# Performance work log

Hardware: AMD Instinct MI355X
Metric: run time of the kernel (lower is better)

The kernel has to match this reference:

```python
import jax, jax.numpy as jnp
import numpy as np

B, S, HID = 1, 2048, 2880
H, KV, D = 64, 8, 64
WINDOW = 128
SCALE = D ** -0.5
NEG_INF = jnp.float32(-1e30)


def _rope_cos_sin():
    # realistic RoPE tables over full head_dim (HF rotate_half convention)
    inv_freq = 1.0 / (10000.0 ** (np.arange(0, D, 2, dtype=np.float32) / D))
    t = np.arange(S, dtype=np.float32)
    freqs = np.outer(t, inv_freq)                      # [S, D/2]
    emb = np.concatenate([freqs, freqs], axis=-1)      # [S, D]
    return jnp.asarray(np.cos(emb))[None], jnp.asarray(np.sin(emb))[None]


def setup_inputs() -> dict:
    key = jax.random.key(0)
    ks = jax.random.split(key, 10)
    cos, sin = _rope_cos_sin()
    sd = lambda fan_in: 1.0 / np.sqrt(fan_in)
    return {
        "hidden_states": jax.random.normal(ks[0], (B, S, HID), jnp.float32),
        "cos": cos, "sin": sin,
        "Wq": jax.random.normal(ks[1], (HID, H * D), jnp.float32) * sd(HID),
        "bq": jax.random.normal(ks[2], (H * D,), jnp.float32) * 0.02,
        "Wk": jax.random.normal(ks[3], (HID, KV * D), jnp.float32) * sd(HID),
        "bk": jax.random.normal(ks[4], (KV * D,), jnp.float32) * 0.02,
        "Wv": jax.random.normal(ks[5], (HID, KV * D), jnp.float32) * sd(HID),
        "bv": jax.random.normal(ks[6], (KV * D,), jnp.float32) * 0.02,
        "Wo": jax.random.normal(ks[7], (H * D, HID), jnp.float32) * sd(H * D),
        "bo": jax.random.normal(ks[8], (HID,), jnp.float32) * 0.02,
        "sinks": jax.random.normal(ks[9], (H,), jnp.float32),
    }


def _rotate_half(x):
    x1, x2 = jnp.split(x, 2, axis=-1)
    return jnp.concatenate([-x2, x1], axis=-1)


def _forward(hidden_states, cos, sin, Wq, bq, Wk, bk, Wv, bv, Wo, bo, sinks):
    q = (hidden_states @ Wq + bq).reshape(B, S, H, D)
    k = (hidden_states @ Wk + bk).reshape(B, S, KV, D)
    v = (hidden_states @ Wv + bv).reshape(B, S, KV, D)
    # RoPE with explicit cos/sin, unsqueeze at head dim (bsnd layout)
    c, s = cos[:, :, None, :], sin[:, :, None, :]
    q = q * c + _rotate_half(q) * s
    k = k * c + _rotate_half(k) * s
    # GQA: expand kv heads to match query heads
    k = jnp.repeat(k, H // KV, axis=2)
    v = jnp.repeat(v, H // KV, axis=2)
    scores = jnp.einsum("bqhd,bkhd->bhqk", q, k) * SCALE  # [B,H,S,S]
    i = jnp.arange(S)[:, None]
    j = jnp.arange(S)[None, :]
    allowed = (j <= i) & (j > i - WINDOW)                  # causal + sliding window
    scores = jnp.where(allowed, scores, NEG_INF)
    # sink-augmented softmax: sinks act as an extra logit per head, dropped after norm
    m = jnp.maximum(scores.max(axis=-1), sinks[None, :, None])  # [B,H,S]
    p = jnp.exp(scores - m[..., None])                      # [B,H,S,S]
    denom = p.sum(axis=-1) + jnp.exp(sinks[None, :, None] - m)  # [B,H,S]
    attn = jnp.einsum("bhqk,bkhd->bqhd", p, v) / denom.transpose(0, 2, 1)[..., None]
    return attn.reshape(B, S, H * D) @ Wo + bo


def reference(hidden_states, cos, sin, Wq, bq, Wk, bk, Wv, bv, Wo, bo, sinks):
    return _forward(hidden_states, cos, sin, Wq, bq, Wk, bk, Wv, bv, Wo, bo, sinks)
```

## Files before the change

### kernel.cpp

```cpp
#include <hip/hip_runtime.h>

typedef unsigned short u16;
typedef __bf16 bf16x8 __attribute__((ext_vector_type(8)));
typedef float f32x4 __attribute__((ext_vector_type(4)));

constexpr int SEQ = 2048;
constexpr int HIDN = 2880;
constexpr int NQKV = 5120;
constexpr float SCALE = 0.125f;
constexpr float NEG_INF = -1e30f;

#define ASM_VMCNT(n)  asm volatile("s_waitcnt vmcnt(" #n ")" ::: "memory")
#define ASM_LGKM(n)   asm volatile("s_waitcnt lgkmcnt(" #n ")" ::: "memory")
#define ASM_BARRIER() asm volatile("s_barrier" ::: "memory")
#define SCHEDBAR()    __builtin_amdgcn_sched_barrier(0)

__device__ __forceinline__ u16 f2bf(float f) {
  unsigned int u = __builtin_bit_cast(unsigned int, f);
  u += 0x7FFFu + ((u >> 16) & 1u);
  return (u16)(u >> 16);
}
__device__ __forceinline__ float bf2f(u16 h) {
  unsigned int u = ((unsigned int)h) << 16;
  return __builtin_bit_cast(float, u);
}
__device__ __forceinline__ void async_load16(const void* g, void* l) {
  __builtin_amdgcn_global_load_lds(
      (const __attribute__((address_space(1))) unsigned int*)g,
      (__attribute__((address_space(3))) unsigned int*)l, 16, 0, 0);
}
__device__ __forceinline__ f32x4 DSR(unsigned addr) {
  f32x4 d;
  asm volatile("ds_read_b128 %0, %1" : "=v"(d) : "v"(addr));
  return d;
}
__device__ __forceinline__ bf16x8 asbf(f32x4 v) { return __builtin_bit_cast(bf16x8, v); }

__global__ __launch_bounds__(256) void conv_f2b(const float* __restrict__ in,
                                                u16* __restrict__ out, long n4) {
  long i = (long)blockIdx.x * 256 + threadIdx.x;
  if (i >= n4) return;
  float4 v = ((const float4*)in)[i];
  u16 o0 = f2bf(v.x), o1 = f2bf(v.y), o2 = f2bf(v.z), o3 = f2bf(v.w);
  out[i * 4 + 0] = o0; out[i * 4 + 1] = o1; out[i * 4 + 2] = o2; out[i * 4 + 3] = o3;
}

__global__ __launch_bounds__(256) void transpose_qkv(const float* __restrict__ Wq,
                                                     const float* __restrict__ Wk,
                                                     const float* __restrict__ Wv,
                                                     u16* __restrict__ out) {
  __shared__ float tile[32][33];
  int c0 = blockIdx.x * 32, r0 = blockIdx.y * 32;
  int tx = threadIdx.x & 31, ty = threadIdx.x >> 5;
  const float* src; int C, cl;
  if (c0 < 4096)      { src = Wq; C = 4096; cl = c0; }
  else if (c0 < 4608) { src = Wk; C = 512;  cl = c0 - 4096; }
  else                { src = Wv; C = 512;  cl = c0 - 4608; }
#pragma unroll
  for (int i = 0; i < 32; i += 8)
    tile[ty + i][tx] = src[(long)(r0 + ty + i) * C + cl + tx];
  __syncthreads();
#pragma unroll
  for (int i = 0; i < 32; i += 8)
    out[(long)(c0 + ty + i) * HIDN + r0 + tx] = f2bf(tile[tx][ty + i]);
}

__global__ __launch_bounds__(256) void transpose_f2b(const float* __restrict__ in,
                                                     u16* __restrict__ out,
                                                     int R, int C, int ostride) {
  __shared__ float tile[32][33];
  int c0 = blockIdx.x * 32, r0 = blockIdx.y * 32;
  int tx = threadIdx.x & 31, ty = threadIdx.x >> 5;
#pragma unroll
  for (int i = 0; i < 32; i += 8)
    tile[ty + i][tx] = in[(long)(r0 + ty + i) * C + c0 + tx];
  __syncthreads();
#pragma unroll
  for (int i = 0; i < 32; i += 8)
    out[(long)(c0 + ty + i) * ostride + r0 + tx] = f2bf(tile[tx][ty + i]);
}

__global__ __launch_bounds__(256) void concat_bias(const float* bq, const float* bk,
                                                   const float* bv, float* out) {
  int t = blockIdx.x * 256 + threadIdx.x;
  if (t < 4096) out[t] = bq[t];
  else if (t < 4608) out[t] = bk[t - 4096];
  else if (t < 5120) out[t] = bv[t - 4608];
}

template <int MODE>
__global__ __launch_bounds__(512, 2) void gemm_8w(const u16* __restrict__ A,
                                                  const u16* __restrict__ Bp,
                                                  const float* __restrict__ bias,
                                                  const float* __restrict__ cosb,
                                                  const float* __restrict__ sinb,
                                                  void* __restrict__ out0,
                                                  float* __restrict__ out1,
                                                  int N, int Kst, int nkt) {
  __shared__ u16 lds[40960];
  const int tid = threadIdx.x, lane = tid & 63, wid = tid >> 6;
  const int wm = wid >> 2, wn = wid & 3;
  const int lr = lane & 15, lk = lane >> 4;

  const int gm = gridDim.x;
  int nwg = gm * gridDim.y;
  int bid = blockIdx.y * gm + blockIdx.x;
  int q8 = nwg >> 3, r8 = nwg & 7;
  int xcd = bid & 7, seq = bid >> 3;
  int swz = (xcd < r8 ? xcd * (q8 + 1) : r8 * (q8 + 1) + (xcd - r8) * q8) + seq;
  const long brow = (long)(swz % gm) * 256;
  const long bcol = (long)(swz / gm) * 256;
  const long kbase = (MODE == 1) ? (long)blockIdx.z * nkt * 32 : 0;

  char* L = (char*)lds;
  const u16* Asrc[2];
  const u16* Bsrc[2];
#pragma unroll
  for (int i = 0; i < 2; ++i) {
    int c = tid + 512 * i;
    long ks = kbase + ((c & 3) ^ ((c >> 3) & 3)) * 8;
    Asrc[i] = A  + (brow + (c >> 2)) * (long)Kst + ks;
    Bsrc[i] = Bp + (bcol + (c >> 2)) * (long)Kst + ks;
  }
  auto stageA = [&](int kt, int ab) {
    char* d = L + ab * 16384;
    async_load16(Asrc[0] + (long)kt * 32, d + tid * 16);
    async_load16(Asrc[1] + (long)kt * 32, d + (tid + 512) * 16);
  };
  auto stageB = [&](int kt, int bb) {
    char* d = L + 49152 + bb * 16384;
    async_load16(Bsrc[0] + (long)kt * 32, d + tid * 16);
    async_load16(Bsrc[1] + (long)kt * 32, d + (tid + 512) * 16);
  };

  const unsigned lds0 = (unsigned)(size_t)L;
  const unsigned xs = (unsigned)((lk ^ ((lr >> 1) & 3)) << 4);
  const unsigned aoff = lds0 + (unsigned)((wm * 128 + lr) * 64) + xs;
  const unsigned boff = lds0 + 49152u + (unsigned)((wn * 64 + lr) * 64) + xs;

  f32x4 acc[8][4] = {};
  stageA(0, 0); stageB(0, 0); stageA(1, 1); stageB(1, 1);
  ASM_VMCNT(4);
  ASM_BARRIER();

  int a3 = 0;
  for (int t = 0; t < nkt; ++t) {
    const unsigned ab = aoff + (unsigned)(a3 * 16384);
    const unsigned bb = boff + (unsigned)((t & 1) * 16384);
    const bool s2 = (t + 2 < nkt);
    const int a3n = (a3 == 2) ? 0 : a3 + 1;
    const int a3s = (a3n == 2) ? 0 : a3n + 1;
    f32x4 a[4], b[4];
#pragma unroll
    for (int mf = 0; mf < 4; ++mf) a[mf] = DSR(ab + mf * 1024u);
#pragma unroll
    for (int nf = 0; nf < 4; ++nf) b[nf] = DSR(bb + nf * 1024u);
    if (s2) stageA(t + 2, a3s);
    ASM_BARRIER();
    ASM_LGKM(0); SCHEDBAR();
    __builtin_amdgcn_s_setprio(1);
#pragma unroll
    for (int mf = 0; mf < 4; ++mf)
#pragma unroll
      for (int nf = 0; nf < 4; ++nf)
        acc[mf][nf] = __builtin_amdgcn_mfma_f32_16x16x32_bf16(asbf(a[mf]), asbf(b[nf]), acc[mf][nf], 0, 0, 0);
    __builtin_amdgcn_s_setprio(0);
    ASM_BARRIER();
#pragma unroll
    for (int mf = 0; mf < 4; ++mf) a[mf] = DSR(ab + (mf + 4) * 1024u);
    if (s2) stageB(t + 2, t & 1);
    ASM_BARRIER();
    ASM_LGKM(0); SCHEDBAR();
    __builtin_amdgcn_s_setprio(1);
#pragma unroll
    for (int mf = 0; mf < 4; ++mf)
#pragma unroll
      for (int nf = 0; nf < 4; ++nf)
        acc[mf + 4][nf] = __builtin_amdgcn_mfma_f32_16x16x32_bf16(asbf(a[mf]), asbf(b[nf]), acc[mf + 4][nf], 0, 0, 0);
    __builtin_amdgcn_s_setprio(0);
    if (s2) { ASM_VMCNT(4); } else { ASM_VMCNT(0); }
    ASM_BARRIER();
    a3 = a3n;
  }

  const int col0 = (int)bcol + wn * 64;
  if (MODE == 0) {
    const bool rope = (col0 < 4608);
#pragma unroll
    for (int mf = 0; mf < 8; ++mf) {
      long row = brow + wm * 128 + mf * 16 + lk * 4;
#pragma unroll
      for (int r = 0; r < 4; ++r) {
        long s = row + r;
        if (rope) {
#pragma unroll
          for (int nf = 0; nf < 2; ++nf) {
            int col = col0 + nf * 16 + lr;
            int d = nf * 16 + lr;
            float c = cosb[s * 64 + d], sn = sinb[s * 64 + d];
            float x1 = acc[mf][nf][r] + bias[col];
            float x2 = acc[mf][nf + 2][r] + bias[col + 32];
            ((u16*)out0)[s * (long)N + col]      = f2bf(x1 * c - x2 * sn);
            ((u16*)out0)[s * (long)N + col + 32] = f2bf(x2 * c + x1 * sn);
          }
        } else {
#pragma unroll
          for (int nf = 0; nf < 4; ++nf) {
            int col = col0 + nf * 16 + lr;
            ((u16*)out0)[s * (long)N + col] = f2bf(acc[mf][nf][r] + bias[col]);
          }
        }
      }
    }
  } else {
    float* o = (blockIdx.z == 0) ? (float*)out0 : out1;
#pragma unroll
    for (int mf = 0; mf < 8; ++mf) {
      long row = brow + wm * 128 + mf * 16 + lk * 4;
#pragma unroll
      for (int nf = 0; nf < 4; ++nf) {
        int col = col0 + nf * 16 + lr;
        if (col < N) {
#pragma unroll
          for (int r = 0; r < 4; ++r)
            o[(row + r) * (long)N + col] = acc[mf][nf][r];
        }
      }
    }
  }
}

__global__ __launch_bounds__(256) void combine_out(const float* __restrict__ P1,
                                                   const float* __restrict__ bias,
                                                   float* __restrict__ out) {
  long i = (long)blockIdx.x * 256 + threadIdx.x;
  if (i >= (long)SEQ * HIDN / 4) return;
  int c4 = (int)(i % (HIDN / 4));
  float4 p0 = ((const float4*)out)[i];
  float4 p1 = ((const float4*)P1)[i];
  float4 b = ((const float4*)bias)[c4];
  float4 r;
  r.x = p0.x + p1.x + b.x; r.y = p0.y + p1.y + b.y;
  r.z = p0.z + p1.z + b.z; r.w = p0.w + p1.w + b.w;
  ((float4*)out)[i] = r;
}

__global__ __launch_bounds__(256, 1) void attn_kernel(const u16* __restrict__ QKV,
                                                      const float* __restrict__ sinks,
                                                      u16* __restrict__ Oa) {
  __shared__ u16 Ks[64 * 64];
  __shared__ u16 Vt[64 * 64];
  __shared__ u16 Ps[4][64 * 72];
  const int tid = threadIdx.x, wid = tid >> 6, lane = tid & 63;
  const int lr = lane & 15, lk = lane >> 4;
  const int i0 = blockIdx.x * 64;
  const int h = blockIdx.y * 4 + wid;
  const int g = h >> 3;

  bf16x8 qf[4][2];
#pragma unroll
  for (int m = 0; m < 4; ++m)
#pragma unroll
    for (int kc = 0; kc < 2; ++kc)
      qf[m][kc] = *(const bf16x8*)&QKV[(long)(i0 + m * 16 + lr) * NQKV + h * 64 + kc * 32 + lk * 8];

  const float sinkh = sinks[h];
  float mrun[4][4], lrun[4][4];
  f32x4 oacc[4][4] = {};
#pragma unroll
  for (int m = 0; m < 4; ++m)
#pragma unroll
    for (int r = 0; r < 4; ++r) { mrun[m][r] = sinkh; lrun[m][r] = 0.f; }

  const int jb0 = (i0 >= 128) ? (i0 - 128) : 0;
  for (int jb = jb0; jb <= i0; jb += 64) {
#pragma unroll
    for (int i = 0; i < 2; ++i) {
      int c = wid * 128 + i * 64 + lane;
      int row = c >> 3, sp = c & 7;
      int ssrc = sp ^ (row & 7);
      async_load16(QKV + (long)(jb + row) * NQKV + 4096 + g * 64 + ssrc * 8,
                   ((char*)Ks) + c * 16);
    }
    {
      int j0 = (tid & 31) * 2, d0 = (tid >> 5) * 8;
      const u16* vp = QKV + (long)(jb + j0) * NQKV + 4608 + g * 64 + d0;
      int4 rv0 = *(const int4*)vp;
      int4 rv1 = *(const int4*)(vp + NQKV);
      const u16* a0 = (const u16*)&rv0;
      const u16* a1 = (const u16*)&rv1;
#pragma unroll
      for (int e = 0; e < 8; ++e) {
        int d = d0 + e;
        unsigned val = (unsigned)a0[e] | ((unsigned)a1[e] << 16);
        int byt = d * 128 + ((((j0 >> 3) ^ (d & 7)) << 4)) + ((j0 & 7) * 2);
        *(unsigned*)((char*)Vt + byt) = val;
      }
    }
    __syncthreads();

    f32x4 sf[4][4] = {};
    __builtin_amdgcn_s_setprio(1);
#pragma unroll
    for (int kc = 0; kc < 2; ++kc) {
      bf16x8 kf[4];
#pragma unroll
      for (int cf = 0; cf < 4; ++cf) {
        int row = cf * 16 + lr;
        kf[cf] = *(const bf16x8*)((const char*)Ks + row * 128 + (((kc * 4 + lk) ^ (lr & 7)) << 4));
      }
#pragma unroll
      for (int m = 0; m < 4; ++m)
#pragma unroll
        for (int cf = 0; cf < 4; ++cf)
          sf[m][cf] = __builtin_amdgcn_mfma_f32_16x16x32_bf16(qf[m][kc], kf[cf], sf[m][cf], 0, 0, 0);
    }
    __builtin_amdgcn_s_setprio(0);

#pragma unroll
    for (int m = 0; m < 4; ++m) {
      float rmax[4];
#pragma unroll
      for (int r = 0; r < 4; ++r) {
        int i = i0 + m * 16 + lk * 4 + r;
        float mx = NEG_INF;
#pragma unroll
        for (int cf = 0; cf < 4; ++cf) {
          int j = jb + cf * 16 + lr;
          float v = sf[m][cf][r] * SCALE;
          bool ok = (j <= i) && (j > i - 128);
          v = ok ? v : NEG_INF;
          sf[m][cf][r] = v;
          mx = fmaxf(mx, v);
        }
#pragma unroll
        for (int off = 1; off < 16; off <<= 1) mx = fmaxf(mx, __shfl_xor(mx, off, 64));
        rmax[r] = mx;
      }
#pragma unroll
      for (int r = 0; r < 4; ++r) {
        float mnew = fmaxf(mrun[m][r], rmax[r]);
        float corr = __expf(mrun[m][r] - mnew);
        mrun[m][r] = mnew;
        float rsum = 0.f;
#pragma unroll
        for (int cf = 0; cf < 4; ++cf) {
          float p = __expf(sf[m][cf][r] - mnew);
          sf[m][cf][r] = p;
          rsum += p;
        }
#pragma unroll
        for (int off = 1; off < 16; off <<= 1) rsum += __shfl_xor(rsum, off, 64);
        lrun[m][r] = lrun[m][r] * corr + rsum;
#pragma unroll
        for (int dn = 0; dn < 4; ++dn) oacc[m][dn][r] *= corr;
      }
    }

#pragma unroll
    for (int m = 0; m < 4; ++m)
#pragma unroll
      for (int cf = 0; cf < 4; ++cf)
#pragma unroll
        for (int r = 0; r < 4; ++r)
          Ps[wid][(m * 16 + lk * 4 + r) * 72 + cf * 16 + lr] = f2bf(sf[m][cf][r]);
    __syncthreads();

    __builtin_amdgcn_s_setprio(1);
#pragma unroll
    for (int kc = 0; kc < 2; ++kc) {
      bf16x8 pf[4], vf[4];
#pragma unroll
      for (int m = 0; m < 4; ++m)
        pf[m] = *(const bf16x8*)&Ps[wid][(m * 16 + lr) * 72 + kc * 32 + lk * 8];
#pragma unroll
      for (int dn = 0; dn < 4; ++dn) {
        int row = dn * 16 + lr;
        vf[dn] = *(const bf16x8*)((const char*)Vt + row * 128 + (((kc * 4 + lk) ^ (lr & 7)) << 4));
      }
#pragma unroll
      for (int m = 0; m < 4; ++m)
#pragma unroll
        for (int dn = 0; dn < 4; ++dn)
          oacc[m][dn] = __builtin_amdgcn_mfma_f32_16x16x32_bf16(pf[m], vf[dn], oacc[m][dn], 0, 0, 0);
    }
    __builtin_amdgcn_s_setprio(0);
    __syncthreads();
  }

#pragma unroll
  for (int m = 0; m < 4; ++m)
#pragma unroll
    for (int r = 0; r < 4; ++r) {
      float denom = lrun[m][r] + __expf(sinkh - mrun[m][r]);
      float inv = 1.f / denom;
      long row = i0 + m * 16 + lk * 4 + r;
#pragma unroll
      for (int dn = 0; dn < 4; ++dn)
        Oa[row * 4096 + h * 64 + dn * 16 + lr] = f2bf(oacc[m][dn][r] * inv);
    }
}

extern "C" void kernel_launch(void* const* d_in, const int* in_sizes, int n_in,
                              void* d_out, int out_size, void* d_ws, size_t ws_size,
                              hipStream_t stream) {
  const float* X    = (const float*)d_in[0];
  const float* cosb = (const float*)d_in[1];
  const float* sinb = (const float*)d_in[2];
  const float* Wq   = (const float*)d_in[3];
  const float* bq   = (const float*)d_in[4];
  const float* Wk   = (const float*)d_in[5];
  const float* bk   = (const float*)d_in[6];
  const float* Wv   = (const float*)d_in[7];
  const float* bv   = (const float*)d_in[8];
  const float* Wo   = (const float*)d_in[9];
  const float* bo   = (const float*)d_in[10];
  const float* sinks = (const float*)d_in[11];

  char* ws = (char*)d_ws;
  size_t off = 0;
  auto alloc = [&](size_t bytes) -> void* {
    void* p = ws + off;
    off += (bytes + 255) & ~(size_t)255;
    return p;
  };
  u16*   Xb    = (u16*)alloc((size_t)SEQ * HIDN * 2);
  u16*   Wqkv  = (u16*)alloc((size_t)NQKV * HIDN * 2);
  u16*   Wot   = (u16*)alloc((size_t)3072 * 4096 * 2);
  float* bqkv  = (float*)alloc((size_t)NQKV * 4);
  u16*   QKV   = (u16*)alloc((size_t)SEQ * NQKV * 2);
  u16*   Ab    = (u16*)alloc((size_t)SEQ * 4096 * 2);
  float* Pt1 = (float*)Wqkv;
  (void)ws_size; (void)in_sizes; (void)n_in; (void)out_size;

  conv_f2b<<<(SEQ * HIDN / 4 + 255) / 256, 256, 0, stream>>>(X, Xb, (long)SEQ * HIDN / 4);
  transpose_qkv<<<dim3(NQKV / 32, HIDN / 32), 256, 0, stream>>>(Wq, Wk, Wv, Wqkv);
  transpose_f2b<<<dim3(HIDN / 32, 4096 / 32), 256, 0, stream>>>(Wo, Wot, 4096, HIDN, 4096);
  concat_bias<<<(NQKV + 255) / 256, 256, 0, stream>>>(bq, bk, bv, bqkv);
  gemm_8w<0><<<dim3(8, 20, 1), 512, 0, stream>>>(Xb, Wqkv, bqkv, cosb, sinb,
                                                 QKV, nullptr, NQKV, HIDN, 90);
  attn_kernel<<<dim3(SEQ / 64, 64 / 4), 256, 0, stream>>>(QKV, sinks, Ab);
  gemm_8w<1><<<dim3(8, 12, 2), 512, 0, stream>>>(Ab, Wot, nullptr, nullptr, nullptr,
                                                 d_out, Pt1, HIDN, 4096, 64);
  combine_out<<<(SEQ * HIDN / 4 + 255) / 256, 256, 0, stream>>>(Pt1, bo, (float*)d_out);
}
```

Before: 246.3 us.

## Replace 256x256 8-wave GEMM with 128x128 double-buffered 4-wave GEMM, drop split-K

Measured after the change: 264.4 us. 1.07x slower.

```diff
diff --git a/kernel.cpp b/kernel.cpp
--- a/kernel.cpp
+++ b/kernel.cpp
@@ -10,11 +10,6 @@
 constexpr float SCALE = 0.125f;
 constexpr float NEG_INF = -1e30f;
 
-#define ASM_VMCNT(n)  asm volatile("s_waitcnt vmcnt(" #n ")" ::: "memory")
-#define ASM_LGKM(n)   asm volatile("s_waitcnt lgkmcnt(" #n ")" ::: "memory")
-#define ASM_BARRIER() asm volatile("s_barrier" ::: "memory")
-#define SCHEDBAR()    __builtin_amdgcn_sched_barrier(0)
-
 __device__ __forceinline__ u16 f2bf(float f) {
   unsigned int u = __builtin_bit_cast(unsigned int, f);
   u += 0x7FFFu + ((u >> 16) & 1u);
@@ -29,12 +24,6 @@
       (const __attribute__((address_space(1))) unsigned int*)g,
       (__attribute__((address_space(3))) unsigned int*)l, 16, 0, 0);
 }
-__device__ __forceinline__ f32x4 DSR(unsigned addr) {
-  f32x4 d;
-  asm volatile("ds_read_b128 %0, %1" : "=v"(d) : "v"(addr));
-  return d;
-}
-__device__ __forceinline__ bf16x8 asbf(f32x4 v) { return __builtin_bit_cast(bf16x8, v); }
 
 __global__ __launch_bounds__(256) void conv_f2b(const float* __restrict__ in,
                                                 u16* __restrict__ out, long n4) {
@@ -89,17 +78,16 @@
 }
 
 template <int MODE>
-__global__ __launch_bounds__(512, 2) void gemm_8w(const u16* __restrict__ A,
+__global__ __launch_bounds__(256, 2) void gemm_db(const u16* __restrict__ A,
                                                   const u16* __restrict__ Bp,
                                                   const float* __restrict__ bias,
                                                   const float* __restrict__ cosb,
                                                   const float* __restrict__ sinb,
                                                   void* __restrict__ out0,
-                                                  float* __restrict__ out1,
                                                   int N, int Kst, int nkt) {
-  __shared__ u16 lds[40960];
+  __shared__ u16 lds[32768];
   const int tid = threadIdx.x, lane = tid & 63, wid = tid >> 6;
-  const int wm = wid >> 2, wn = wid & 3;
+  const int wm = wid >> 1, wn = wid & 1;
   const int lr = lane & 15, lk = lane >> 4;
 
   const int gm = gridDim.x;
@@ -108,87 +96,70 @@
   int q8 = nwg >> 3, r8 = nwg & 7;
   int xcd = bid & 7, seq = bid >> 3;
   int swz = (xcd < r8 ? xcd * (q8 + 1) : r8 * (q8 + 1) + (xcd - r8) * q8) + seq;
-  const long brow = (long)(swz % gm) * 256;
-  const long bcol = (long)(swz / gm) * 256;
-  const long kbase = (MODE == 1) ? (long)blockIdx.z * nkt * 32 : 0;
+  const long brow = (long)(swz % gm) * 128;
+  const long bcol = (long)(swz / gm) * 128;
 
   char* L = (char*)lds;
-  const u16* Asrc[2];
-  const u16* Bsrc[2];
+  const int kc8 = ((tid & 3) ^ ((tid >> 3) & 3)) * 8;
+  const u16* As[2];
+  const u16* Bs[2];
 #pragma unroll
   for (int i = 0; i < 2; ++i) {
-    int c = tid + 512 * i;
-    long ks = kbase + ((c & 3) ^ ((c >> 3) & 3)) * 8;
-    Asrc[i] = A  + (brow + (c >> 2)) * (long)Kst + ks;
-    Bsrc[i] = Bp + (bcol + (c >> 2)) * (long)Kst + ks;
+    int c = tid + 256 * i;
+    As[i] = A  + (brow + (c >> 2)) * (long)Kst + kc8;
+    Bs[i] = Bp + (bcol + (c >> 2)) * (long)Kst + kc8;
   }
-  auto stageA = [&](int kt, int ab) {
-    char* d = L + ab * 16384;
-    async_load16(Asrc[0] + (long)kt * 32, d + tid * 16);
-    async_load16(Asrc[1] + (long)kt * 32, d + (tid + 512) * 16);
+  auto stage = [&](int kt, int b) {
+    char* d = L + b * 32768;
+    long ko = (long)kt * 64;
+#pragma unroll
+    for (int i = 0; i < 2; ++i) {
+      async_load16(As[i] + ko,      d +         i * 4096 + tid * 16);
+      async_load16(As[i] + ko + 32, d +  8192 + i * 4096 + tid * 16);
+      async_load16(Bs[i] + ko,      d + 16384 + i * 4096 + tid * 16);
+      async_load16(Bs[i] + ko + 32, d + 24576 + i * 4096 + tid * 16);
+    }
   };
-  auto stageB = [&](int kt, int bb) {
-    char* d = L + 49152 + bb * 16384;
-    async_load16(Bsrc[0] + (long)kt * 32, d + tid * 16);
-    async_load16(Bsrc[1] + (long)kt * 32, d + (tid + 512) * 16);
-  };
-
-  const unsigned lds0 = (unsigned)(size_t)L;
-  const unsigned xs = (unsigned)((lk ^ ((lr >> 1) & 3)) << 4);
-  const unsigned aoff = lds0 + (unsigned)((wm * 128 + lr) * 64) + xs;
-  const unsigned boff = lds0 + 49152u + (unsigned)((wn * 64 + lr) * 64) + xs;
-
-  f32x4 acc[8][4] = {};
-  stageA(0, 0); stageB(0, 0); stageA(1, 1); stageB(1, 1);
-  ASM_VMCNT(4);
-  ASM_BARRIER();
-
-  int a3 = 0;
+
+  const int phys = (lk ^ ((lr >> 1) & 3)) << 4;
+  const int arow = (wm * 64 + lr) * 64 + phys;
+  const int brow_ = (wn * 64 + lr) * 64 + phys;
+
+  f32x4 acc[4][4] = {};
+  stage(0, 0);
+  __syncthreads();
+
   for (int t = 0; t < nkt; ++t) {
-    const unsigned ab = aoff + (unsigned)(a3 * 16384);
-    const unsigned bb = boff + (unsigned)((t & 1) * 16384);
-    const bool s2 = (t + 2 < nkt);
-    const int a3n = (a3 == 2) ? 0 : a3 + 1;
-    const int a3s = (a3n == 2) ? 0 : a3n + 1;
-    f32x4 a[4], b[4];
-#pragma unroll
-    for (int mf = 0; mf < 4; ++mf) a[mf] = DSR(ab + mf * 1024u);
-#pragma unroll
-    for (int nf = 0; nf < 4; ++nf) b[nf] = DSR(bb + nf * 1024u);
-    if (s2) stageA(t + 2, a3s);
-    ASM_BARRIER();
-    ASM_LGKM(0); SCHEDBAR();
-    __builtin_amdgcn_s_setprio(1);
-#pragma unroll
-    for (int mf = 0; mf < 4; ++mf)
-#pragma unroll
-      for (int nf = 0; nf < 4; ++nf)
-        acc[mf][nf] = __builtin_amdgcn_mfma_f32_16x16x32_bf16(asbf(a[mf]), asbf(b[nf]), acc[mf][nf], 0, 0, 0);
-    __builtin_amdgcn_s_setprio(0);
-    ASM_BARRIER();
-#pragma unroll
-    for (int mf = 0; mf < 4; ++mf) a[mf] = DSR(ab + (mf + 4) * 1024u);
-    if (s2) stageB(t + 2, t & 1);
-    ASM_BARRIER();
-    ASM_LGKM(0); SCHEDBAR();
-    __builtin_amdgcn_s_setprio(1);
-#pragma unroll
-    for (int mf = 0; mf < 4; ++mf)
-#pragma unroll
-      for (int nf = 0; nf < 4; ++nf)
-        acc[mf + 4][nf] = __builtin_amdgcn_mfma_f32_16x16x32_bf16(asbf(a[mf]), asbf(b[nf]), acc[mf + 4][nf], 0, 0, 0);
-    __builtin_amdgcn_s_setprio(0);
-    if (s2) { ASM_VMCNT(4); } else { ASM_VMCNT(0); }
-    ASM_BARRIER();
-    a3 = a3n;
+    const char* Lb = L + (t & 1) * 32768;
+    bf16x8 a0[4], b0[4], a1[4], b1[4];
+#pragma unroll
+    for (int m = 0; m < 4; ++m) a0[m] = *(const bf16x8*)(Lb + arow + m * 1024);
+#pragma unroll
+    for (int n = 0; n < 4; ++n) b0[n] = *(const bf16x8*)(Lb + 16384 + brow_ + n * 1024);
+#pragma unroll
+    for (int m = 0; m < 4; ++m) a1[m] = *(const bf16x8*)(Lb + 8192 + arow + m * 1024);
+#pragma unroll
+    for (int n = 0; n < 4; ++n) b1[n] = *(const bf16x8*)(Lb + 24576 + brow_ + n * 1024);
+    if (t + 1 < nkt) stage(t + 1, (t & 1) ^ 1);
+#pragma unroll
+    for (int m = 0; m < 4; ++m)
+#pragma unroll
+      for (int n = 0; n < 4; ++n)
+        acc[m][n] = __builtin_amdgcn_mfma_f32_16x16x32_bf16(a0[m], b0[n], acc[m][n], 0, 0, 0);
+#pragma unroll
+    for (int m = 0; m < 4; ++m)
+#pragma unroll
+      for (int n = 0; n < 4; ++n)
+        acc[m][n] = __builtin_amdgcn_mfma_f32_16x16x32_bf16(a1[m], b1[n], acc[m][n], 0, 0, 0);
+    __syncthreads();
   }
 
   const int col0 = (int)bcol + wn * 64;
   if (MODE == 0) {
     const bool rope = (col0 < 4608);
 #pragma unroll
-    for (int mf = 0; mf < 8; ++mf) {
-      long row = brow + wm * 128 + mf * 16 + lk * 4;
+    for (int mf = 0; mf < 4; ++mf) {
+      long row = brow + wm * 64 + mf * 16 + lk * 4;
 #pragma unroll
       for (int r = 0; r < 4; ++r) {
         long s = row + r;
@@ -213,36 +184,21 @@
       }
     }
   } else {
-    float* o = (blockIdx.z == 0) ? (float*)out0 : out1;
-#pragma unroll
-    for (int mf = 0; mf < 8; ++mf) {
-      long row = brow + wm * 128 + mf * 16 + lk * 4;
+#pragma unroll
+    for (int mf = 0; mf < 4; ++mf) {
+      long row = brow + wm * 64 + mf * 16 + lk * 4;
 #pragma unroll
       for (int nf = 0; nf < 4; ++nf) {
         int col = col0 + nf * 16 + lr;
         if (col < N) {
+          float bv = bias[col];
 #pragma unroll
           for (int r = 0; r < 4; ++r)
-            o[(row + r) * (long)N + col] = acc[mf][nf][r];
+            ((float*)out0)[(row + r) * (long)N + col] = acc[mf][nf][r] + bv;
         }
       }
     }
   }
-}
-
-__global__ __launch_bounds__(256) void combine_out(const float* __restrict__ P1,
-                                                   const float* __restrict__ bias,
-                                                   float* __restrict__ out) {
-  long i = (long)blockIdx.x * 256 + threadIdx.x;
-  if (i >= (long)SEQ * HIDN / 4) return;
-  int c4 = (int)(i % (HIDN / 4));
-  float4 p0 = ((const float4*)out)[i];
-  float4 p1 = ((const float4*)P1)[i];
-  float4 b = ((const float4*)bias)[c4];
-  float4 r;
-  r.x = p0.x + p1.x + b.x; r.y = p0.y + p1.y + b.y;
-  r.z = p0.z + p1.z + b.z; r.w = p0.w + p1.w + b.w;
-  ((float4*)out)[i] = r;
 }
 
 __global__ __launch_bounds__(256, 1) void attn_kernel(const u16* __restrict__ QKV,
@@ -426,21 +382,19 @@
   };
   u16*   Xb    = (u16*)alloc((size_t)SEQ * HIDN * 2);
   u16*   Wqkv  = (u16*)alloc((size_t)NQKV * HIDN * 2);
-  u16*   Wot   = (u16*)alloc((size_t)3072 * 4096 * 2);
+  u16*   Wot   = (u16*)alloc((size_t)2944 * 4096 * 2);
   float* bqkv  = (float*)alloc((size_t)NQKV * 4);
   u16*   QKV   = (u16*)alloc((size_t)SEQ * NQKV * 2);
   u16*   Ab    = (u16*)alloc((size_t)SEQ * 4096 * 2);
-  float* Pt1 = (float*)Wqkv;
   (void)ws_size; (void)in_sizes; (void)n_in; (void)out_size;
 
   conv_f2b<<<(SEQ * HIDN / 4 + 255) / 256, 256, 0, stream>>>(X, Xb, (long)SEQ * HIDN / 4);
   transpose_qkv<<<dim3(NQKV / 32, HIDN / 32), 256, 0, stream>>>(Wq, Wk, Wv, Wqkv);
   transpose_f2b<<<dim3(HIDN / 32, 4096 / 32), 256, 0, stream>>>(Wo, Wot, 4096, HIDN, 4096);
   concat_bias<<<(NQKV + 255) / 256, 256, 0, stream>>>(bq, bk, bv, bqkv);
-  gemm_8w<0><<<dim3(8, 20, 1), 512, 0, stream>>>(Xb, Wqkv, bqkv, cosb, sinb,
-                                                 QKV, nullptr, NQKV, HIDN, 90);
+  gemm_db<0><<<dim3(16, 40), 256, 0, stream>>>(Xb, Wqkv, bqkv, cosb, sinb,
+                                               QKV, NQKV, HIDN, 45);
   attn_kernel<<<dim3(SEQ / 64, 64 / 4), 256, 0, stream>>>(QKV, sinks, Ab);
-  gemm_8w<1><<<dim3(8, 12, 2), 512, 0, stream>>>(Ab, Wot, nullptr, nullptr, nullptr,
-                                                 d_out, Pt1, HIDN, 4096, 64);
-  combine_out<<<(SEQ * HIDN / 4 + 255) / 256, 256, 0, stream>>>(Pt1, bo, (float*)d_out);
-}
+  gemm_db<1><<<dim3(16, 23), 256, 0, stream>>>(Ab, Wot, bo, nullptr, nullptr,
+                                               d_out, HIDN, 4096, 64);
+}
```

## Restructure GEMM main loop to 64-wide K tiles with 128KB double-buffered LDS

Applied to the files above, without the earlier changes.

After: 329.0 us. 33.6% more time.

```diff
diff --git a/kernel.cpp b/kernel.cpp
--- a/kernel.cpp
+++ b/kernel.cpp
@@ -89,15 +89,16 @@
 }
 
 template <int MODE>
-__global__ __launch_bounds__(512, 2) void gemm_8w(const u16* __restrict__ A,
-                                                  const u16* __restrict__ Bp,
-                                                  const float* __restrict__ bias,
-                                                  const float* __restrict__ cosb,
-                                                  const float* __restrict__ sinb,
-                                                  void* __restrict__ out0,
-                                                  float* __restrict__ out1,
-                                                  int N, int Kst, int nkt) {
-  __shared__ u16 lds[40960];
+__global__ __launch_bounds__(512, 2) void gemm8p(const u16* __restrict__ A,
+                                                 const u16* __restrict__ Bp,
+                                                 const float* __restrict__ bias,
+                                                 const float* __restrict__ cosb,
+                                                 const float* __restrict__ sinb,
+                                                 void* __restrict__ out0,
+                                                 float* __restrict__ out1,
+                                                 int N, int Kst, int nkt) {
+  extern __shared__ u16 ldsx[];
+  char* Lc = (char*)ldsx;
   const int tid = threadIdx.x, lane = tid & 63, wid = tid >> 6;
   const int wm = wid >> 2, wn = wid & 3;
   const int lr = lane & 15, lk = lane >> 4;
@@ -110,77 +111,112 @@
   int swz = (xcd < r8 ? xcd * (q8 + 1) : r8 * (q8 + 1) + (xcd - r8) * q8) + seq;
   const long brow = (long)(swz % gm) * 256;
   const long bcol = (long)(swz / gm) * 256;
-  const long kbase = (MODE == 1) ? (long)blockIdx.z * nkt * 32 : 0;
-
-  char* L = (char*)lds;
-  const u16* Asrc[2];
-  const u16* Bsrc[2];
-#pragma unroll
-  for (int i = 0; i < 2; ++i) {
-    int c = tid + 512 * i;
-    long ks = kbase + ((c & 3) ^ ((c >> 3) & 3)) * 8;
-    Asrc[i] = A  + (brow + (c >> 2)) * (long)Kst + ks;
-    Bsrc[i] = Bp + (bcol + (c >> 2)) * (long)Kst + ks;
-  }
-  auto stageA = [&](int kt, int ab) {
-    char* d = L + ab * 16384;
-    async_load16(Asrc[0] + (long)kt * 32, d + tid * 16);
-    async_load16(Asrc[1] + (long)kt * 32, d + (tid + 512) * 16);
+  const long kbase = (MODE == 1) ? (long)blockIdx.z * nkt * 64 : 0;
+
+  const int row0 = tid >> 3;
+  const int k0 = ((tid & 7) ^ (row0 & 7)) * 8;
+  const u16* Abase = A  + (brow + row0) * (long)Kst + kbase + k0;
+  const u16* Bbase = Bp + (bcol + row0) * (long)Kst + kbase + k0;
+  auto stage1 = [&](int kt, int r) {
+    char* dst = Lc + (kt & 1) * 65536 + r * 16384 + tid * 16;
+    const u16* s = (r < 2) ? (Abase + (long)r * 128 * Kst + (long)kt * 64)
+                           : (Bbase + (long)(r - 2) * 128 * Kst + (long)kt * 64);
+    async_load16(s, dst);
+    async_load16(s + 64 * (long)Kst, dst + 8192);
   };
-  auto stageB = [&](int kt, int bb) {
-    char* d = L + 49152 + bb * 16384;
-    async_load16(Bsrc[0] + (long)kt * 32, d + tid * 16);
-    async_load16(Bsrc[1] + (long)kt * 32, d + (tid + 512) * 16);
+
+  const unsigned lds0 = (unsigned)(size_t)Lc;
+  const unsigned aReg = lds0 + (unsigned)(wm * 16384);
+  const unsigned bReg = lds0 + 32768u + (unsigned)((wn >> 1) * 16384);
+  const unsigned bColOff = (unsigned)((wn & 1) * 64 * 128);
+  unsigned px[2];
+#pragma unroll
+  for (int ks = 0; ks < 2; ++ks) px[ks] = (unsigned)(((ks * 4 + lk) ^ (lr & 7)) << 4);
+
+  f32x4 acc[8][4] = {};
+  auto rdA = [&](int d, int mh, f32x4 (*af)[2]) {
+#pragma unroll
+    for (int mf = 0; mf < 4; ++mf)
+#pragma unroll
+      for (int ks = 0; ks < 2; ++ks)
+        af[mf][ks] = DSR(aReg + d * 65536u + (unsigned)(((mh * 4 + mf) * 16 + lr) * 128) + px[ks]);
   };
-
-  const unsigned lds0 = (unsigned)(size_t)L;
-  const unsigned xs = (unsigned)((lk ^ ((lr >> 1) & 3)) << 4);
-  const unsigned aoff = lds0 + (unsigned)((wm * 128 + lr) * 64) + xs;
-  const unsigned boff = lds0 + 49152u + (unsigned)((wn * 64 + lr) * 64) + xs;
-
-  f32x4 acc[8][4] = {};
-  stageA(0, 0); stageB(0, 0); stageA(1, 1); stageB(1, 1);
+  auto rdB = [&](int d, int nh, f32x4 (*bx)[2]) {
+#pragma unroll
+    for (int nf = 0; nf < 2; ++nf)
+#pragma unroll
+      for (int ks = 0; ks < 2; ++ks)
+        bx[nf][ks] = DSR(bReg + d * 65536u + bColOff + (unsigned)(((nh * 2 + nf) * 16 + lr) * 128) + px[ks]);
+  };
+  auto quad = [&](int mb, int nb, f32x4 (*af)[2], f32x4 (*bx)[2]) {
+    __builtin_amdgcn_s_setprio(1);
+#pragma unroll
+    for (int ks = 0; ks < 2; ++ks)
+#pragma unroll
+      for (int mf = 0; mf < 4; ++mf)
+#pragma unroll
+        for (int nf = 0; nf < 2; ++nf)
+          acc[mb + mf][nb + nf] = __builtin_amdgcn_mfma_f32_16x16x32_bf16(
+              asbf(af[mf][ks]), asbf(bx[nf][ks]), acc[mb + mf][nb + nf], 0, 0, 0);
+    __builtin_amdgcn_s_setprio(0);
+  };
+
+  stage1(0, 0); stage1(0, 1); stage1(0, 2); stage1(0, 3);
+  if (nkt > 1) { stage1(1, 2); stage1(1, 3); }
   ASM_VMCNT(4);
   ASM_BARRIER();
 
-  int a3 = 0;
-  for (int t = 0; t < nkt; ++t) {
-    const unsigned ab = aoff + (unsigned)(a3 * 16384);
-    const unsigned bb = boff + (unsigned)((t & 1) * 16384);
-    const bool s2 = (t + 2 < nkt);
-    const int a3n = (a3 == 2) ? 0 : a3 + 1;
-    const int a3s = (a3n == 2) ? 0 : a3n + 1;
-    f32x4 a[4], b[4];
-#pragma unroll
-    for (int mf = 0; mf < 4; ++mf) a[mf] = DSR(ab + mf * 1024u);
-#pragma unroll
-    for (int nf = 0; nf < 4; ++nf) b[nf] = DSR(bb + nf * 1024u);
-    if (s2) stageA(t + 2, a3s);
-    ASM_BARRIER();
+  f32x4 af[4][2], b0[2][2], b1[2][2];
+  const int niter = nkt >> 1;
+  for (int it = 0; it < niter; ++it) {
+    const int E = 2 * it, O = E + 1;
+    const bool sE2 = (E + 2 < nkt), sO2 = (O + 2 < nkt);
+    rdA(0, 0, af); rdB(0, 0, b0);
+    stage1(O, 0);
+    ASM_BARRIER(); ASM_LGKM(0); SCHEDBAR();
+    quad(0, 0, af, b0);
+    ASM_BARRIER();
+    rdB(0, 1, b1);
+    stage1(O, 1);
+    ASM_BARRIER(); ASM_LGKM(0); SCHEDBAR();
+    quad(0, 2, af, b1);
+    ASM_BARRIER();
+    rdA(0, 1, af);
+    if (sE2) stage1(E + 2, 2);
+    ASM_BARRIER(); ASM_LGKM(0); SCHEDBAR();
+    quad(4, 2, af, b1);
+    ASM_BARRIER();
+    if (sE2) { stage1(E + 2, 3); ASM_VMCNT(4); } else { ASM_VMCNT(0); }
+    ASM_BARRIER(); SCHEDBAR();
+    quad(4, 0, af, b0);
+    ASM_BARRIER();
+    rdA(1, 0, af); rdB(1, 0, b0);
+    if (sE2) stage1(E + 2, 0);
+    ASM_BARRIER(); ASM_LGKM(0); SCHEDBAR();
+    quad(0, 0, af, b0);
+    ASM_BARRIER();
+    rdB(1, 1, b1);
+    if (sE2) stage1(E + 2, 1);
+    ASM_BARRIER(); ASM_LGKM(0); SCHEDBAR();
+    quad(0, 2, af, b1);
+    ASM_BARRIER();
+    rdA(1, 1, af);
+    if (sO2) stage1(O + 2, 2);
+    ASM_BARRIER(); ASM_LGKM(0); SCHEDBAR();
+    quad(4, 2, af, b1);
+    ASM_BARRIER();
+    if (sO2) { stage1(O + 2, 3); ASM_VMCNT(4); } else { ASM_VMCNT(0); }
+    ASM_BARRIER(); SCHEDBAR();
+    quad(4, 0, af, b0);
+    ASM_BARRIER();
+  }
+  if (nkt & 1) {
+    rdA(0, 0, af); rdB(0, 0, b0); rdB(0, 1, b1);
     ASM_LGKM(0); SCHEDBAR();
-    __builtin_amdgcn_s_setprio(1);
-#pragma unroll
-    for (int mf = 0; mf < 4; ++mf)
-#pragma unroll
-      for (int nf = 0; nf < 4; ++nf)
-        acc[mf][nf] = __builtin_amdgcn_mfma_f32_16x16x32_bf16(asbf(a[mf]), asbf(b[nf]), acc[mf][nf], 0, 0, 0);
-    __builtin_amdgcn_s_setprio(0);
-    ASM_BARRIER();
-#pragma unroll
-    for (int mf = 0; mf < 4; ++mf) a[mf] = DSR(ab + (mf + 4) * 1024u);
-    if (s2) stageB(t + 2, t & 1);
-    ASM_BARRIER();
+    quad(0, 0, af, b0); quad(0, 2, af, b1);
+    rdA(0, 1, af);
     ASM_LGKM(0); SCHEDBAR();
-    __builtin_amdgcn_s_setprio(1);
-#pragma unroll
-    for (int mf = 0; mf < 4; ++mf)
-#pragma unroll
-      for (int nf = 0; nf < 4; ++nf)
-        acc[mf + 4][nf] = __builtin_amdgcn_mfma_f32_16x16x32_bf16(asbf(a[mf]), asbf(b[nf]), acc[mf + 4][nf], 0, 0, 0);
-    __builtin_amdgcn_s_setprio(0);
-    if (s2) { ASM_VMCNT(4); } else { ASM_VMCNT(0); }
-    ASM_BARRIER();
-    a3 = a3n;
+    quad(4, 2, af, b1); quad(4, 0, af, b0);
   }
 
   const int col0 = (int)bcol + wn * 64;
@@ -417,6 +453,15 @@
   const float* bo   = (const float*)d_in[10];
   const float* sinks = (const float*)d_in[11];
 
+  static bool attrDone = false;
+  if (!attrDone) {
+    hipFuncSetAttribute((const void*)gemm8p<0>,
+                        hipFuncAttributeMaxDynamicSharedMemorySize, 131072);
+    hipFuncSetAttribute((const void*)gemm8p<1>,
+                        hipFuncAttributeMaxDynamicSharedMemorySize, 131072);
+    attrDone = true;
+  }
+
   char* ws = (char*)d_ws;
   size_t off = 0;
   auto alloc = [&](size_t bytes) -> void* {
@@ -437,10 +482,10 @@
   transpose_qkv<<<dim3(NQKV / 32, HIDN / 32), 256, 0, stream>>>(Wq, Wk, Wv, Wqkv);
   transpose_f2b<<<dim3(HIDN / 32, 4096 / 32), 256, 0, stream>>>(Wo, Wot, 4096, HIDN, 4096);
   concat_bias<<<(NQKV + 255) / 256, 256, 0, stream>>>(bq, bk, bv, bqkv);
-  gemm_8w<0><<<dim3(8, 20, 1), 512, 0, stream>>>(Xb, Wqkv, bqkv, cosb, sinb,
-                                                 QKV, nullptr, NQKV, HIDN, 90);
+  gemm8p<0><<<dim3(8, 20, 1), 512, 131072, stream>>>(Xb, Wqkv, bqkv, cosb, sinb,
+                                                     QKV, nullptr, NQKV, HIDN, 45);
   attn_kernel<<<dim3(SEQ / 64, 64 / 4), 256, 0, stream>>>(QKV, sinks, Ab);
-  gemm_8w<1><<<dim3(8, 12, 2), 512, 0, stream>>>(Ab, Wot, nullptr, nullptr, nullptr,
-                                                 d_out, Pt1, HIDN, 4096, 64);
+  gemm8p<1><<<dim3(8, 12, 2), 512, 131072, stream>>>(Ab, Wot, nullptr, nullptr, nullptr,
+                                                     d_out, Pt1, HIDN, 4096, 32);
   combine_out<<<(SEQ * HIDN / 4 + 255) / 256, 256, 0, stream>>>(Pt1, bo, (float*)d_out);
 }
```
